# Kernel optimization log

Hardware: AMD Instinct MI355X
Metric: run time of the kernel (lower is better)

Reference implementation:

```python
import jax, jax.numpy as jnp
import numpy as np
from jax import lax

EPS = 1e-06
S = 0.025
ALPHA = 0.98
DELTA = 2.0
R = 0.5


def setup_inputs() -> dict:
    key = jax.random.key(0)
    # magnitude spectrogram: [batch, freq, time], nonnegative
    x = jax.random.uniform(key, (32, 256, 4096), dtype=jnp.float32)
    return {"x": x}


def reference(x):
    # x: [B, F, T]; EMA smoother runs over the time axis (last dim).
    # m_0 = s*x_0 ; m_t = (1-s)*m_{t-1} + s*x_t  (init carry 0 reproduces m_0 = s*x_0)
    xt = jnp.moveaxis(x, 2, 0)  # [T, B, F]

    def step(m, frame):
        m = (1.0 - S) * m + S * frame
        return m, m

    _, M = lax.scan(step, jnp.zeros_like(xt[0]), xt)  # [T, B, F]
    M = jnp.moveaxis(M, 0, 2)  # [B, F, T]
    # power-law compression fused elementwise
    return (x / (M + EPS) ** ALPHA + DELTA) ** R - DELTA ** R
```

## Files before the change

### kernel.cpp

```cpp
#include <hip/hip_runtime.h>


constexpr int T_LEN = 4096;
constexpr int LANES = 64;
constexpr int NSUB  = 16;
constexpr int WAVES_PER_BLK = 4;
constexpr int NTHR  = LANES * WAVES_PER_BLK;

constexpr float EPSF = 1e-6f;
constexpr float SF   = 0.025f;
constexpr float A1F  = 0.975f;

constexpr double dA1   = 0.975;
constexpr double dA2   = dA1 * dA1;
constexpr double dA4   = dA2 * dA2;
constexpr double dA8   = dA4 * dA4;
constexpr double dA16  = dA8 * dA8;
constexpr double dA32  = dA16 * dA16;
constexpr double dA64  = dA32 * dA32;
constexpr double dA128 = dA64 * dA64;
constexpr double dA256 = dA128 * dA128;

__global__ __launch_bounds__(NTHR) void pcen_wave_kernel(
    const float* __restrict__ x, float* __restrict__ out, int rows)
{
    const int lane = threadIdx.x & 63;
    const int wave = threadIdx.x >> 6;
    const int row  = blockIdx.x * WAVES_PER_BLK + wave;
    if (row >= rows) return;

    const long long base = (long long)row * T_LEN;
    const float4* __restrict__ px   = (const float4*)(x + base);
    float4* __restrict__       pout = (float4*)(out + base);

    const float cA4   = (float)dA4;
    const float cA8   = (float)dA8;
    const float cA16  = (float)dA16;
    const float cA32  = (float)dA32;
    const float cA64  = (float)dA64;
    const float cA128 = (float)dA128;
    const float cA256 = (float)dA256;

    float flane = 1.0f;
    if (lane & 1)  flane *= cA4;
    if (lane & 2)  flane *= cA8;
    if (lane & 4)  flane *= cA16;
    if (lane & 8)  flane *= cA32;
    if (lane & 16) flane *= cA64;
    if (lane & 32) flane *= cA128;

    const float SQRT_D = 1.41421356237309515f;

    float4 d[NSUB];
#pragma unroll
    for (int s = 0; s < NSUB; ++s) d[s] = px[s * LANES + lane];

    asm volatile("" ::: "memory");

    float Sv[NSUB];
#pragma unroll
    for (int s = 0; s < NSUB; ++s) {
        float m = SF * d[s].x;
        m = fmaf(A1F, m, SF * d[s].y);
        m = fmaf(A1F, m, SF * d[s].z);
        m = fmaf(A1F, m, SF * d[s].w);
        Sv[s] = m;
    }

#pragma unroll
    for (int s = 0; s < NSUB; ++s) {
        float tt;
        tt = __shfl_up(Sv[s], 1,  64); if (lane >= 1)  Sv[s] = fmaf(cA4,   tt, Sv[s]);
        tt = __shfl_up(Sv[s], 2,  64); if (lane >= 2)  Sv[s] = fmaf(cA8,   tt, Sv[s]);
        tt = __shfl_up(Sv[s], 4,  64); if (lane >= 4)  Sv[s] = fmaf(cA16,  tt, Sv[s]);
        tt = __shfl_up(Sv[s], 8,  64); if (lane >= 8)  Sv[s] = fmaf(cA32,  tt, Sv[s]);
        tt = __shfl_up(Sv[s], 16, 64); if (lane >= 16) Sv[s] = fmaf(cA64,  tt, Sv[s]);
        tt = __shfl_up(Sv[s], 32, 64); if (lane >= 32) Sv[s] = fmaf(cA128, tt, Sv[s]);
    }

    float carry = 0.0f;
#pragma unroll
    for (int s = 0; s < NSUB; ++s) {
        float excl = __shfl_up(Sv[s], 1, 64);
        if (lane == 0) excl = 0.0f;
        float last = __shfl(Sv[s], 63, 64);

        float m = fmaf(flane, carry, excl);
        carry   = fmaf(cA256, carry, last);

        float4 v = d[s];
        float4 o;
        m = fmaf(A1F, m, SF * v.x);
        o.x = __builtin_amdgcn_sqrtf(
                  fmaf(v.x, __builtin_amdgcn_exp2f(
                      -0.98f * __builtin_amdgcn_logf(m + EPSF)), 2.0f)) - SQRT_D;
        m = fmaf(A1F, m, SF * v.y);
        o.y = __builtin_amdgcn_sqrtf(
                  fmaf(v.y, __builtin_amdgcn_exp2f(
                      -0.98f * __builtin_amdgcn_logf(m + EPSF)), 2.0f)) - SQRT_D;
        m = fmaf(A1F, m, SF * v.z);
        o.z = __builtin_amdgcn_sqrtf(
                  fmaf(v.z, __builtin_amdgcn_exp2f(
                      -0.98f * __builtin_amdgcn_logf(m + EPSF)), 2.0f)) - SQRT_D;
        m = fmaf(A1F, m, SF * v.w);
        o.w = __builtin_amdgcn_sqrtf(
                  fmaf(v.w, __builtin_amdgcn_exp2f(
                      -0.98f * __builtin_amdgcn_logf(m + EPSF)), 2.0f)) - SQRT_D;

        pout[s * LANES + lane] = o;
    }
}

extern "C" void kernel_launch(void* const* d_in, const int* in_sizes, int n_in,
                              void* d_out, int out_size, void* d_ws, size_t ws_size,
                              hipStream_t stream) {
    const float* x = (const float*)d_in[0];
    float* out = (float*)d_out;
    const int rows = in_sizes[0] / T_LEN;
    const int blocks = (rows + WAVES_PER_BLK - 1) / WAVES_PER_BLK;
    pcen_wave_kernel<<<dim3(blocks), dim3(NTHR), 0, stream>>>(x, out, rows);
}
```

Before: 235.2 us.

## Process four rows per wave with double-buffered loads and nontemporal stores

Each wave now handles four rows and uses two register buffers, so the next row's global loads are issued while the current row is scanned and stored. Output stores use nontemporal hints to avoid polluting the cache. The grid becomes four times smaller (512 blocks) and register pressure roughly doubles from two 16-float4 buffers. That may reduce occupancy and leave fewer blocks to spread across the CUs.

New measurement: 236.9 us. About the same (+0.7%).

```diff
diff --git a/kernel.cpp b/kernel.cpp
--- a/kernel.cpp
+++ b/kernel.cpp
@@ -1,9 +1,12 @@
 #include <hip/hip_runtime.h>
 
+
+typedef float f32x4 __attribute__((ext_vector_type(4)));
 
 constexpr int T_LEN = 4096;
 constexpr int LANES = 64;
 constexpr int NSUB  = 16;
+constexpr int ROWS_PW = 4;
 constexpr int WAVES_PER_BLK = 4;
 constexpr int NTHR  = LANES * WAVES_PER_BLK;
 
@@ -26,12 +29,9 @@
 {
     const int lane = threadIdx.x & 63;
     const int wave = threadIdx.x >> 6;
-    const int row  = blockIdx.x * WAVES_PER_BLK + wave;
-    if (row >= rows) return;
-
-    const long long base = (long long)row * T_LEN;
-    const float4* __restrict__ px   = (const float4*)(x + base);
-    float4* __restrict__       pout = (float4*)(out + base);
+    const int wid  = blockIdx.x * WAVES_PER_BLK + wave;
+    const int row0 = wid * ROWS_PW;
+    if (row0 >= rows) return;
 
     const float cA4   = (float)dA4;
     const float cA8   = (float)dA8;
@@ -51,63 +51,87 @@
 
     const float SQRT_D = 1.41421356237309515f;
 
-    float4 d[NSUB];
+    auto load_row = [&](float4* dst, int r) {
+        const float4* p = (const float4*)(x + (long long)r * T_LEN);
 #pragma unroll
-    for (int s = 0; s < NSUB; ++s) d[s] = px[s * LANES + lane];
+        for (int s = 0; s < NSUB; ++s) dst[s] = p[s * LANES + lane];
+        asm volatile("" ::: "memory");
+    };
 
-    asm volatile("" ::: "memory");
+    auto scan_store = [&](const float4* d, int r) {
+        float4* po = (float4*)(out + (long long)r * T_LEN);
 
-    float Sv[NSUB];
+        float Sv[NSUB];
 #pragma unroll
-    for (int s = 0; s < NSUB; ++s) {
-        float m = SF * d[s].x;
-        m = fmaf(A1F, m, SF * d[s].y);
-        m = fmaf(A1F, m, SF * d[s].z);
-        m = fmaf(A1F, m, SF * d[s].w);
-        Sv[s] = m;
-    }
+        for (int s = 0; s < NSUB; ++s) {
+            float m = SF * d[s].x;
+            m = fmaf(A1F, m, SF * d[s].y);
+            m = fmaf(A1F, m, SF * d[s].z);
+            m = fmaf(A1F, m, SF * d[s].w);
+            Sv[s] = m;
+        }
 
 #pragma unroll
-    for (int s = 0; s < NSUB; ++s) {
-        float tt;
-        tt = __shfl_up(Sv[s], 1,  64); if (lane >= 1)  Sv[s] = fmaf(cA4,   tt, Sv[s]);
-        tt = __shfl_up(Sv[s], 2,  64); if (lane >= 2)  Sv[s] = fmaf(cA8,   tt, Sv[s]);
-        tt = __shfl_up(Sv[s], 4,  64); if (lane >= 4)  Sv[s] = fmaf(cA16,  tt, Sv[s]);
-        tt = __shfl_up(Sv[s], 8,  64); if (lane >= 8)  Sv[s] = fmaf(cA32,  tt, Sv[s]);
-        tt = __shfl_up(Sv[s], 16, 64); if (lane >= 16) Sv[s] = fmaf(cA64,  tt, Sv[s]);
-        tt = __shfl_up(Sv[s], 32, 64); if (lane >= 32) Sv[s] = fmaf(cA128, tt, Sv[s]);
-    }
+        for (int s = 0; s < NSUB; ++s) {
+            float tt;
+            tt = __shfl_up(Sv[s], 1,  64); if (lane >= 1)  Sv[s] = fmaf(cA4,   tt, Sv[s]);
+            tt = __shfl_up(Sv[s], 2,  64); if (lane >= 2)  Sv[s] = fmaf(cA8,   tt, Sv[s]);
+            tt = __shfl_up(Sv[s], 4,  64); if (lane >= 4)  Sv[s] = fmaf(cA16,  tt, Sv[s]);
+            tt = __shfl_up(Sv[s], 8,  64); if (lane >= 8)  Sv[s] = fmaf(cA32,  tt, Sv[s]);
+            tt = __shfl_up(Sv[s], 16, 64); if (lane >= 16) Sv[s] = fmaf(cA64,  tt, Sv[s]);
+            tt = __shfl_up(Sv[s], 32, 64); if (lane >= 32) Sv[s] = fmaf(cA128, tt, Sv[s]);
+        }
 
-    float carry = 0.0f;
+        float carry = 0.0f;
 #pragma unroll
-    for (int s = 0; s < NSUB; ++s) {
-        float excl = __shfl_up(Sv[s], 1, 64);
-        if (lane == 0) excl = 0.0f;
-        float last = __shfl(Sv[s], 63, 64);
+        for (int s = 0; s < NSUB; ++s) {
+            float excl = __shfl_up(Sv[s], 1, 64);
+            if (lane == 0) excl = 0.0f;
+            float last = __shfl(Sv[s], 63, 64);
 
-        float m = fmaf(flane, carry, excl);
-        carry   = fmaf(cA256, carry, last);
+            float m = fmaf(flane, carry, excl);
+            carry   = fmaf(cA256, carry, last);
 
-        float4 v = d[s];
-        float4 o;
-        m = fmaf(A1F, m, SF * v.x);
-        o.x = __builtin_amdgcn_sqrtf(
-                  fmaf(v.x, __builtin_amdgcn_exp2f(
-                      -0.98f * __builtin_amdgcn_logf(m + EPSF)), 2.0f)) - SQRT_D;
-        m = fmaf(A1F, m, SF * v.y);
-        o.y = __builtin_amdgcn_sqrtf(
-                  fmaf(v.y, __builtin_amdgcn_exp2f(
-                      -0.98f * __builtin_amdgcn_logf(m + EPSF)), 2.0f)) - SQRT_D;
-        m = fmaf(A1F, m, SF * v.z);
-        o.z = __builtin_amdgcn_sqrtf(
-                  fmaf(v.z, __builtin_amdgcn_exp2f(
-                      -0.98f * __builtin_amdgcn_logf(m + EPSF)), 2.0f)) - SQRT_D;
-        m = fmaf(A1F, m, SF * v.w);
-        o.w = __builtin_amdgcn_sqrtf(
-                  fmaf(v.w, __builtin_amdgcn_exp2f(
-                      -0.98f * __builtin_amdgcn_logf(m + EPSF)), 2.0f)) - SQRT_D;
+            float4 v = d[s];
+            float4 o;
+            m = fmaf(A1F, m, SF * v.x);
+            o.x = __builtin_amdgcn_sqrtf(
+                      fmaf(v.x, __builtin_amdgcn_exp2f(
+                          -0.98f * __builtin_amdgcn_logf(m + EPSF)), 2.0f)) - SQRT_D;
+            m = fmaf(A1F, m, SF * v.y);
+            o.y = __builtin_amdgcn_sqrtf(
+                      fmaf(v.y, __builtin_amdgcn_exp2f(
+                          -0.98f * __builtin_amdgcn_logf(m + EPSF)), 2.0f)) - SQRT_D;
+            m = fmaf(A1F, m, SF * v.z);
+            o.z = __builtin_amdgcn_sqrtf(
+                      fmaf(v.z, __builtin_amdgcn_exp2f(
+                          -0.98f * __builtin_amdgcn_logf(m + EPSF)), 2.0f)) - SQRT_D;
+            m = fmaf(A1F, m, SF * v.w);
+            o.w = __builtin_amdgcn_sqrtf(
+                      fmaf(v.w, __builtin_amdgcn_exp2f(
+                          -0.98f * __builtin_amdgcn_logf(m + EPSF)), 2.0f)) - SQRT_D;
 
-        pout[s * LANES + lane] = o;
+            f32x4 ov = {o.x, o.y, o.z, o.w};
+            __builtin_nontemporal_store(ov, (f32x4*)(po + s * LANES + lane));
+        }
+    };
+
+    float4 bufA[NSUB], bufB[NSUB];
+
+    if (row0 + ROWS_PW <= rows) {
+        load_row(bufA, row0);
+        load_row(bufB, row0 + 1);
+        scan_store(bufA, row0);
+        load_row(bufA, row0 + 2);
+        scan_store(bufB, row0 + 1);
+        load_row(bufB, row0 + 3);
+        scan_store(bufA, row0 + 2);
+        scan_store(bufB, row0 + 3);
+    } else {
+        for (int r = row0; r < rows; ++r) {
+            load_row(bufA, r);
+            scan_store(bufA, r);
+        }
     }
 }
 
@@ -117,6 +141,7 @@
     const float* x = (const float*)d_in[0];
     float* out = (float*)d_out;
     const int rows = in_sizes[0] / T_LEN;
-    const int blocks = (rows + WAVES_PER_BLK - 1) / WAVES_PER_BLK;
+    const int rows_per_blk = ROWS_PW * WAVES_PER_BLK;
+    const int blocks = (rows + rows_per_blk - 1) / rows_per_blk;
     pcen_wave_kernel<<<dim3(blocks), dim3(NTHR), 0, stream>>>(x, out, rows);
 }
```

## Software-pipeline half-row loads with inline asm across four rows per wave

Applied to the files above, without the earlier changes.

Each wave now processes four rows in halves of 2048 elements. It double-buffers the next half's global loads, issued through inline asm dwordx4 with explicit vmcnt waits, so they overlap with the scan and transcendental math of the current half. The grid shrinks fourfold to a persistent-style layout, which trades occupancy for load-compute overlap. A fallback loop handles row counts that are not divisible.

Result: no change. 238.7 us (+1.5%).

```diff
diff --git a/kernel.cpp b/kernel.cpp
--- a/kernel.cpp
+++ b/kernel.cpp
@@ -1,11 +1,14 @@
 #include <hip/hip_runtime.h>
 
 
-constexpr int T_LEN = 4096;
-constexpr int LANES = 64;
-constexpr int NSUB  = 16;
+typedef float f32x4 __attribute__((ext_vector_type(4)));
+
+constexpr int T_LEN      = 4096;
+constexpr int HALF_ELEMS = 2048;
+constexpr int SUBS       = 8;
+constexpr int NROWS_PW   = 4;
 constexpr int WAVES_PER_BLK = 4;
-constexpr int NTHR  = LANES * WAVES_PER_BLK;
+constexpr int NTHR       = 256;
 
 constexpr float EPSF = 1e-6f;
 constexpr float SF   = 0.025f;
@@ -21,17 +24,25 @@
 constexpr double dA128 = dA64 * dA64;
 constexpr double dA256 = dA128 * dA128;
 
-__global__ __launch_bounds__(NTHR) void pcen_wave_kernel(
+#define GLOAD(dst, base, imm)                                        \
+    asm volatile("global_load_dwordx4 %0, %1, off offset:" #imm     \
+                 : "=v"(dst) : "v"(base))
+
+#define VMWAIT8()                                  \
+    do {                                           \
+        asm volatile("s_waitcnt vmcnt(8)");        \
+        __builtin_amdgcn_sched_barrier(0);         \
+    } while (0)
+
+#define SBAR() __builtin_amdgcn_sched_barrier(0)
+
+__global__ __launch_bounds__(NTHR) void pcen_pipe_kernel(
     const float* __restrict__ x, float* __restrict__ out, int rows)
 {
     const int lane = threadIdx.x & 63;
     const int wave = threadIdx.x >> 6;
-    const int row  = blockIdx.x * WAVES_PER_BLK + wave;
-    if (row >= rows) return;
-
-    const long long base = (long long)row * T_LEN;
-    const float4* __restrict__ px   = (const float4*)(x + base);
-    float4* __restrict__       pout = (float4*)(out + base);
+    const int NW   = gridDim.x * WAVES_PER_BLK;
+    const int wid  = blockIdx.x * WAVES_PER_BLK + wave;
 
     const float cA4   = (float)dA4;
     const float cA8   = (float)dA8;
@@ -51,63 +62,102 @@
 
     const float SQRT_D = 1.41421356237309515f;
 
-    float4 d[NSUB];
+    auto issue = [&](f32x4* buf, int r, int h) {
+        const float* b0 = x + (long long)r * T_LEN + h * HALF_ELEMS + (lane << 2);
+        const float* b1 = b0 + 1024;
+        GLOAD(buf[0], b0, 0);
+        GLOAD(buf[1], b0, 1024);
+        GLOAD(buf[2], b0, 2048);
+        GLOAD(buf[3], b0, 3072);
+        GLOAD(buf[4], b1, 0);
+        GLOAD(buf[5], b1, 1024);
+        GLOAD(buf[6], b1, 2048);
+        GLOAD(buf[7], b1, 3072);
+        SBAR();
+    };
+
+    auto process = [&](const f32x4* d, int r, int h, float carry) -> float {
+        float Sv[SUBS];
 #pragma unroll
-    for (int s = 0; s < NSUB; ++s) d[s] = px[s * LANES + lane];
+        for (int s = 0; s < SUBS; ++s) {
+            float m = SF * d[s].x;
+            m = fmaf(A1F, m, SF * d[s].y);
+            m = fmaf(A1F, m, SF * d[s].z);
+            m = fmaf(A1F, m, SF * d[s].w);
+            Sv[s] = m;
+        }
+#pragma unroll
+        for (int s = 0; s < SUBS; ++s) {
+            float tt;
+            tt = __shfl_up(Sv[s], 1,  64); if (lane >= 1)  Sv[s] = fmaf(cA4,   tt, Sv[s]);
+            tt = __shfl_up(Sv[s], 2,  64); if (lane >= 2)  Sv[s] = fmaf(cA8,   tt, Sv[s]);
+            tt = __shfl_up(Sv[s], 4,  64); if (lane >= 4)  Sv[s] = fmaf(cA16,  tt, Sv[s]);
+            tt = __shfl_up(Sv[s], 8,  64); if (lane >= 8)  Sv[s] = fmaf(cA32,  tt, Sv[s]);
+            tt = __shfl_up(Sv[s], 16, 64); if (lane >= 16) Sv[s] = fmaf(cA64,  tt, Sv[s]);
+            tt = __shfl_up(Sv[s], 32, 64); if (lane >= 32) Sv[s] = fmaf(cA128, tt, Sv[s]);
+        }
+        float* po = out + (long long)r * T_LEN + h * HALF_ELEMS + (lane << 2);
+#pragma unroll
+        for (int s = 0; s < SUBS; ++s) {
+            float excl = __shfl_up(Sv[s], 1, 64);
+            if (lane == 0) excl = 0.0f;
+            float last = __shfl(Sv[s], 63, 64);
 
-    asm volatile("" ::: "memory");
+            float m = fmaf(flane, carry, excl);
+            carry   = fmaf(cA256, carry, last);
 
-    float Sv[NSUB];
+            f32x4 v = d[s];
+            f32x4 o;
+            m = fmaf(A1F, m, SF * v.x);
+            o.x = __builtin_amdgcn_sqrtf(
+                      fmaf(v.x, __builtin_amdgcn_exp2f(
+                          -0.98f * __builtin_amdgcn_logf(m + EPSF)), 2.0f)) - SQRT_D;
+            m = fmaf(A1F, m, SF * v.y);
+            o.y = __builtin_amdgcn_sqrtf(
+                      fmaf(v.y, __builtin_amdgcn_exp2f(
+                          -0.98f * __builtin_amdgcn_logf(m + EPSF)), 2.0f)) - SQRT_D;
+            m = fmaf(A1F, m, SF * v.z);
+            o.z = __builtin_amdgcn_sqrtf(
+                      fmaf(v.z, __builtin_amdgcn_exp2f(
+                          -0.98f * __builtin_amdgcn_logf(m + EPSF)), 2.0f)) - SQRT_D;
+            m = fmaf(A1F, m, SF * v.w);
+            o.w = __builtin_amdgcn_sqrtf(
+                      fmaf(v.w, __builtin_amdgcn_exp2f(
+                          -0.98f * __builtin_amdgcn_logf(m + EPSF)), 2.0f)) - SQRT_D;
+
+            *(f32x4*)(po + s * 256) = o;
+        }
+        SBAR();
+        return carry;
+    };
+
+    f32x4 A[SUBS], B[SUBS];
+    const int r0 = wid;
+
+    if (r0 + 3 * NW < rows) {
+        const int r[4] = { r0, r0 + NW, r0 + 2 * NW, r0 + 3 * NW };
+        issue(A, r[0], 0);
 #pragma unroll
-    for (int s = 0; s < NSUB; ++s) {
-        float m = SF * d[s].x;
-        m = fmaf(A1F, m, SF * d[s].y);
-        m = fmaf(A1F, m, SF * d[s].z);
-        m = fmaf(A1F, m, SF * d[s].w);
-        Sv[s] = m;
-    }
-
+        for (int k = 0; k < 4; ++k) {
+            issue(B, r[k], 1);
+            VMWAIT8();
+            float carry = process(A, r[k], 0, 0.0f);
+            if (k < 3) issue(A, r[k + 1], 0);
+            VMWAIT8();
+            (void)process(B, r[k], 1, carry);
+        }
+    } else {
+        for (int rr = r0; rr < rows; rr += NW) {
+            float carry = 0.0f;
+            f32x4 tmp[SUBS];
+            for (int h = 0; h < 2; ++h) {
+                const float* pb = x + (long long)rr * T_LEN + h * HALF_ELEMS + (lane << 2);
 #pragma unroll
-    for (int s = 0; s < NSUB; ++s) {
-        float tt;
-        tt = __shfl_up(Sv[s], 1,  64); if (lane >= 1)  Sv[s] = fmaf(cA4,   tt, Sv[s]);
-        tt = __shfl_up(Sv[s], 2,  64); if (lane >= 2)  Sv[s] = fmaf(cA8,   tt, Sv[s]);
-        tt = __shfl_up(Sv[s], 4,  64); if (lane >= 4)  Sv[s] = fmaf(cA16,  tt, Sv[s]);
-        tt = __shfl_up(Sv[s], 8,  64); if (lane >= 8)  Sv[s] = fmaf(cA32,  tt, Sv[s]);
-        tt = __shfl_up(Sv[s], 16, 64); if (lane >= 16) Sv[s] = fmaf(cA64,  tt, Sv[s]);
-        tt = __shfl_up(Sv[s], 32, 64); if (lane >= 32) Sv[s] = fmaf(cA128, tt, Sv[s]);
-    }
-
-    float carry = 0.0f;
-#pragma unroll
-    for (int s = 0; s < NSUB; ++s) {
-        float excl = __shfl_up(Sv[s], 1, 64);
-        if (lane == 0) excl = 0.0f;
-        float last = __shfl(Sv[s], 63, 64);
-
-        float m = fmaf(flane, carry, excl);
-        carry   = fmaf(cA256, carry, last);
-
-        float4 v = d[s];
-        float4 o;
-        m = fmaf(A1F, m, SF * v.x);
-        o.x = __builtin_amdgcn_sqrtf(
-                  fmaf(v.x, __builtin_amdgcn_exp2f(
-                      -0.98f * __builtin_amdgcn_logf(m + EPSF)), 2.0f)) - SQRT_D;
-        m = fmaf(A1F, m, SF * v.y);
-        o.y = __builtin_amdgcn_sqrtf(
-                  fmaf(v.y, __builtin_amdgcn_exp2f(
-                      -0.98f * __builtin_amdgcn_logf(m + EPSF)), 2.0f)) - SQRT_D;
-        m = fmaf(A1F, m, SF * v.z);
-        o.z = __builtin_amdgcn_sqrtf(
-                  fmaf(v.z, __builtin_amdgcn_exp2f(
-                      -0.98f * __builtin_amdgcn_logf(m + EPSF)), 2.0f)) - SQRT_D;
-        m = fmaf(A1F, m, SF * v.w);
-        o.w = __builtin_amdgcn_sqrtf(
-                  fmaf(v.w, __builtin_amdgcn_exp2f(
-                      -0.98f * __builtin_amdgcn_logf(m + EPSF)), 2.0f)) - SQRT_D;
-
-        pout[s * LANES + lane] = o;
+                for (int s = 0; s < SUBS; ++s)
+                    tmp[s] = *(const f32x4*)(pb + s * 256);
+                carry = process(tmp, rr, h, h ? carry : 0.0f);
+            }
+        }
     }
 }
 
@@ -117,6 +167,7 @@
     const float* x = (const float*)d_in[0];
     float* out = (float*)d_out;
     const int rows = in_sizes[0] / T_LEN;
-    const int blocks = (rows + WAVES_PER_BLK - 1) / WAVES_PER_BLK;
-    pcen_wave_kernel<<<dim3(blocks), dim3(NTHR), 0, stream>>>(x, out, rows);
+    const int rows_per_blk = NROWS_PW * WAVES_PER_BLK;
+    const int blocks = (rows + rows_per_blk - 1) / rows_per_blk;
+    pcen_pipe_kernel<<<dim3(blocks), dim3(NTHR), 0, stream>>>(x, out, rows);
 }
```
